# Kernel optimization log

Measured on AMD Instinct MI355X. Metric: run time of the kernel, lower is better.

Reference implementation:

```python
import jax, jax.numpy as jnp
import numpy as np

B, N, M = 8192, 64, 32          # batch, num_fields, embedding_dim
D = N * (N - 1) // 2            # 2016 pairwise-interaction rows of theta
OUT = 1024                      # block_out_dim
BN_EPS = 1e-5


def setup_inputs() -> dict:
    key = jax.random.key(0)
    k0, k1, k2, k3 = jax.random.split(key, 4)
    inputs = jax.random.normal(k0, (B, N * M), dtype=jnp.float32)
    W_z = jax.random.normal(k1, (N, N, M), dtype=jnp.float32) * 0.05
    theta = jax.random.normal(k2, (D, N), dtype=jnp.float32) * 0.05
    w_affine = jax.random.normal(k3, (OUT, N + D), dtype=jnp.float32) * 0.02
    b_affine = jnp.zeros((OUT,), dtype=jnp.float32)
    gamma = jnp.ones((OUT,), dtype=jnp.float32)
    beta = jnp.zeros((OUT,), dtype=jnp.float32)
    return {"inputs": inputs, "W_z": W_z, "theta": theta,
            "w_affine": w_affine, "b_affine": b_affine,
            "gamma": gamma, "beta": beta}


def reference(inputs, W_z, theta, w_affine, b_affine, gamma, beta):
    b = inputs.shape[0]
    x = inputs.reshape(b, N, M)                      # [B, N, M]
    # lz term: full quadratic form with W_z
    lz = jnp.einsum('bnm,dnm->bd', x, W_z)           # [B, N]
    # lp term: algebraically identical to einsum('bdnm,bdnm->bd') over
    # delta = einsum('bnm,dn->bdnm'): lp[b,d] = sum_n theta[d,n]^2 * sum_m x[b,n,m]^2
    x_sq = jnp.sum(x * x, axis=-1)                   # [B, N]
    lp = x_sq @ (theta * theta).T                    # [B, D]
    out = jnp.concatenate([lz, lp], axis=1)          # [B, N+D]
    out = out @ w_affine.T + b_affine                # [B, OUT]
    # BatchNorm1d in training mode (batch statistics, biased variance)
    mean = jnp.mean(out, axis=0)
    var = jnp.var(out, axis=0)
    out = (out - mean) * jax.lax.rsqrt(var + BN_EPS) * gamma + beta
    return out
```

## Files before the change

### kernel.cpp

```cpp
#include <hip/hip_runtime.h>
#include <stdint.h>

#define NROWS 8192
#define KX    2048
#define KA    2112
#define NF    64
#define DD    2016
#define WCOLS 2080
#define ODIM  1024
#define BN_EPS 1e-5f

#define A1_OT 32
#define A2_DC 8
#define A2_DPC 252
#define A2_OT 16

#define CONV_RPB 4
#define CONV_NB  (NROWS / CONV_RPB)
#define RED_NB   (ODIM * NF / 256)

#define A1A2_A1N 256
#define A1A2_A2E 768
#define A1A2_TOT 776

#define GBM 64
#define GBN 128
#define NT (KA / 32)

using f32x4  = __attribute__((ext_vector_type(4))) float;
using bf16x8 = __attribute__((ext_vector_type(8))) short;

__device__ __forceinline__ short f2bf(float x) {
    uint32_t u = __float_as_uint(x);
    uint32_t r = (u + 0x7FFFu + ((u >> 16) & 1u)) >> 16;
    return (short)r;
}

__device__ __forceinline__ void gload16(const void* g, void* l) {
    __builtin_amdgcn_global_load_lds(
        (const __attribute__((address_space(1))) uint32_t*)g,
        (__attribute__((address_space(3))) uint32_t*)l, 16, 0, 0);
}

#define MFMA_BF16 __builtin_amdgcn_mfma_f32_16x16x32_bf16

__global__ __launch_bounds__(256) void conv_kern(const float* __restrict__ X,
                                                 short* __restrict__ Xa,
                                                 const float* __restrict__ partials,
                                                 short* __restrict__ Aw) {
    const int t = threadIdx.x;
    const int b = blockIdx.x;
    if (b < CONV_NB) {
#pragma unroll
        for (int r = 0; r < CONV_RPB; ++r) {
            const int row = b * CONV_RPB + r;
            const float4* xr = reinterpret_cast<const float4*>(X + (size_t)row * KX);
            float4 v0 = xr[t * 2];
            float4 v1 = xr[t * 2 + 1];
            bf16x8 s;
            s[0] = f2bf(v0.x); s[1] = f2bf(v0.y); s[2] = f2bf(v0.z); s[3] = f2bf(v0.w);
            s[4] = f2bf(v1.x); s[5] = f2bf(v1.y); s[6] = f2bf(v1.z); s[7] = f2bf(v1.w);
            short* outr = Xa + (size_t)row * KA;
            reinterpret_cast<bf16x8*>(outr)[t] = s;
            float sq = v0.x*v0.x + v0.y*v0.y + v0.z*v0.z + v0.w*v0.w
                     + v1.x*v1.x + v1.y*v1.y + v1.z*v1.z + v1.w*v1.w;
            sq += __shfl_xor(sq, 1);
            sq += __shfl_xor(sq, 2);
            if ((t & 3) == 0) outr[KX + (t >> 2)] = f2bf(sq - 32.0f);
        }
    } else {
        const int idx = (b - CONV_NB) * 256 + t;
        const int o = idx >> 6, n = idx & 63;
        float s = 0.f;
#pragma unroll
        for (int c = 0; c < A2_DC; ++c)
            s += partials[((size_t)c * ODIM + o) * NF + n];
        Aw[(size_t)o * KA + KX + n] = f2bf(s);
    }
}

__global__ __launch_bounds__(256) void a1a2_kern(short* __restrict__ Aw,
                                                 const float* __restrict__ Wa,
                                                 const float* __restrict__ Wz,
                                                 const float* __restrict__ theta,
                                                 float* __restrict__ partials,
                                                 float* __restrict__ sums) {
    const int bid = blockIdx.x;
    const int t = threadIdx.x;
    __shared__ __align__(16) float smem[4096];

    if (bid >= A1A2_A2E) {
        sums[(bid - A1A2_A2E) * 256 + t] = 0.f;
        return;
    }
    if (bid < A1A2_A1N) {
        const int k = (bid & 7) * 256 + t;
        const int o0 = (bid >> 3) * A1_OT;
        for (int idx = t; idx < A1_OT * 64; idx += 256)
            smem[idx] = Wa[(size_t)(o0 + (idx >> 6)) * WCOLS + (idx & 63)];
        float wz[64];
#pragma unroll
        for (int d = 0; d < 64; ++d) wz[d] = Wz[(size_t)d * KX + k];
        __syncthreads();
#pragma unroll 2
        for (int j = 0; j < A1_OT; ++j) {
            const float* war = &smem[j * 64];
            float acc = 0.f;
#pragma unroll
            for (int d = 0; d < 64; ++d) acc += war[d] * wz[d];
            Aw[(size_t)(o0 + j) * KA + k] = f2bf(acc);
        }
    } else {
        const int b = bid - A1A2_A1N;
        const int n = t & 63;
        const int g = t >> 6;
        const int chunk = b & 7;
        const int o0 = (b >> 3) * A2_OT;
        const int d0 = chunk * A2_DPC;
        float* waT = smem;
        for (int idx = t; idx < A2_OT * A2_DPC; idx += 256) {
            const int j = idx / A2_DPC, dd = idx - j * A2_DPC;
            waT[idx] = Wa[(size_t)(o0 + j) * WCOLS + NF + d0 + dd];
        }
        __syncthreads();
        float acc[A2_OT];
#pragma unroll
        for (int j = 0; j < A2_OT; ++j) acc[j] = 0.f;
        for (int i = g; i < A2_DPC; i += 4) {
            float th = theta[(size_t)(d0 + i) * NF + n];
            float th2 = th * th;
#pragma unroll
            for (int j = 0; j < A2_OT; ++j)
                acc[j] += waT[j * A2_DPC + i] * th2;
        }
        __syncthreads();
        float* red = smem;
#pragma unroll
        for (int j = 0; j < A2_OT; ++j) red[(g * A2_OT + j) * 64 + n] = acc[j];
        __syncthreads();
#pragma unroll
        for (int k2 = 0; k2 < A2_OT * 64 / 256; ++k2) {
            const int idx = t + k2 * 256;
            const int ol = idx >> 6, nn = idx & 63;
            float s = red[(0 * A2_OT + ol) * 64 + nn] + red[(1 * A2_OT + ol) * 64 + nn]
                    + red[(2 * A2_OT + ol) * 64 + nn] + red[(3 * A2_OT + ol) * 64 + nn];
            partials[((size_t)chunk * ODIM + o0 + ol) * NF + nn] = s;
        }
    }
}

__global__ __launch_bounds__(128) void gemm_kern(const short* __restrict__ Xa,
                                                 const short* __restrict__ Aw,
                                                 float* __restrict__ C,
                                                 float* __restrict__ sums) {
    __shared__ __align__(16) short As[3][GBM * 32];
    __shared__ __align__(16) short Bs[3][GBN * 32];
    const int tid  = threadIdx.x;
    const int lane = tid & 63;
    const int wc   = tid >> 6;
    const int bm = blockIdx.x * GBM;
    const int bn = blockIdx.y * GBN;

    f32x4 acc[4][4] = {};

    const short* gA[2]; int lA[2];
#pragma unroll
    for (int i = 0; i < 2; ++i) {
        const int c = tid + i * 128;
        const int r = c >> 2, q = (c & 3) ^ ((r >> 1) & 3);
        gA[i] = Xa + (size_t)(bm + r) * KA + q * 8;
        lA[i] = c * 8;
    }
    const short* gB[4]; int lB[4];
#pragma unroll
    for (int i = 0; i < 4; ++i) {
        const int c = tid + i * 128;
        const int r = c >> 2, q = (c & 3) ^ ((r >> 1) & 3);
        gB[i] = Aw + (size_t)(bn + r) * KA + q * 8;
        lB[i] = c * 8;
    }

    const int lq = lane >> 4;
    int offA[4], offB[4];
#pragma unroll
    for (int m = 0; m < 4; ++m) {
        int ra = m * 16 + (lane & 15);
        offA[m] = ra * 32 + (lq ^ ((ra >> 1) & 3)) * 8;
        int rb = wc * 64 + m * 16 + (lane & 15);
        offB[m] = rb * 32 + (lq ^ ((rb >> 1) & 3)) * 8;
    }

#define STAGE(buf, kt) do {                         \
        const int ko_ = (kt) * 32;                  \
        gload16(gA[0] + ko_, &As[buf][lA[0]]);      \
        gload16(gA[1] + ko_, &As[buf][lA[1]]);      \
        gload16(gB[0] + ko_, &Bs[buf][lB[0]]);      \
        gload16(gB[1] + ko_, &Bs[buf][lB[1]]);      \
        gload16(gB[2] + ko_, &Bs[buf][lB[2]]);      \
        gload16(gB[3] + ko_, &Bs[buf][lB[3]]);      \
    } while (0)

#define TILE(cbuf, sbuf, kt) do {                                          \
        if ((kt) + 2 < NT) STAGE(sbuf, (kt) + 2);                          \
        bf16x8 a_[4], b_[4];                                               \
        _Pragma("unroll")                                                  \
        for (int m = 0; m < 4; ++m)                                        \
            a_[m] = *reinterpret_cast<const bf16x8*>(&As[cbuf][offA[m]]);  \
        _Pragma("unroll")                                                  \
        for (int n = 0; n < 4; ++n)                                        \
            b_[n] = *reinterpret_cast<const bf16x8*>(&Bs[cbuf][offB[n]]);  \
        asm volatile("s_waitcnt lgkmcnt(0)" ::: "memory");                 \
        __builtin_amdgcn_sched_barrier(0);                                 \
        _Pragma("unroll")                                                  \
        for (int m = 0; m < 4; ++m)                                        \
            _Pragma("unroll")                                              \
            for (int n = 0; n < 4; ++n)                                    \
                acc[m][n] = MFMA_BF16(a_[m], b_[n], acc[m][n], 0, 0, 0);   \
        if ((kt) + 2 < NT)                                                 \
            asm volatile("s_waitcnt vmcnt(6)" ::: "memory");               \
        else if ((kt) + 1 < NT)                                            \
            asm volatile("s_waitcnt vmcnt(0)" ::: "memory");               \
        __builtin_amdgcn_s_barrier();                                      \
    } while (0)

    STAGE(0, 0);
    STAGE(1, 1);
    asm volatile("s_waitcnt vmcnt(6)" ::: "memory");
    __builtin_amdgcn_s_barrier();

    for (int kt = 0; kt < NT; kt += 3) {
        TILE(0, 2, kt);
        TILE(1, 0, kt + 1);
        TILE(2, 1, kt + 2);
    }
#undef TILE
#undef STAGE

    const int rlo = (lane >> 4) * 4;
    const int cl  = lane & 15;
#pragma unroll
    for (int n = 0; n < 4; ++n) {
        const int col = bn + wc * 64 + n * 16 + cl;
        float s = 0.f, q = 0.f;
#pragma unroll
        for (int m = 0; m < 4; ++m) {
            const int rowb = bm + m * 16 + rlo;
#pragma unroll
            for (int r2 = 0; r2 < 4; ++r2) {
                float v = acc[m][n][r2];
                C[(size_t)(rowb + r2) * ODIM + col] = v;
                s += v; q += v * v;
            }
        }
        s += __shfl_xor(s, 16); s += __shfl_xor(s, 32);
        q += __shfl_xor(q, 16); q += __shfl_xor(q, 32);
        if (lane < 16) {
            atomicAdd(&sums[col], s);
            atomicAdd(&sums[ODIM + col], q);
        }
    }
}

__global__ __launch_bounds__(256) void bn_apply(float* __restrict__ C,
                                                const float* __restrict__ sums,
                                                const float* __restrict__ gamma,
                                                const float* __restrict__ beta) {
    const int g = blockIdx.x * 256 + threadIdx.x;
    const int c4 = g & (ODIM / 4 - 1);
    const int row0 = g >> 8;
    const float inv = 1.0f / (float)NROWS;
    float4 sc, sh;
    {
        float4 s0 = reinterpret_cast<const float4*>(sums)[c4];
        float4 q0 = reinterpret_cast<const float4*>(sums + ODIM)[c4];
        float4 gm = reinterpret_cast<const float4*>(gamma)[c4];
        float4 bt = reinterpret_cast<const float4*>(beta)[c4];
        float m, v;
        m = s0.x * inv; v = q0.x * inv - m * m; sc.x = gm.x * rsqrtf(v + BN_EPS); sh.x = bt.x - m * sc.x;
        m = s0.y * inv; v = q0.y * inv - m * m; sc.y = gm.y * rsqrtf(v + BN_EPS); sh.y = bt.y - m * sc.y;
        m = s0.z * inv; v = q0.z * inv - m * m; sc.z = gm.z * rsqrtf(v + BN_EPS); sh.z = bt.z - m * sc.z;
        m = s0.w * inv; v = q0.w * inv - m * m; sc.w = gm.w * rsqrtf(v + BN_EPS); sh.w = bt.w - m * sc.w;
    }
#pragma unroll
    for (int r = 0; r < 4; ++r) {
        const size_t i = (size_t)(row0 + r * 2048) * (ODIM / 4) + c4;
        float4 v = reinterpret_cast<const float4*>(C)[i];
        v.x = v.x * sc.x + sh.x;
        v.y = v.y * sc.y + sh.y;
        v.z = v.z * sc.z + sh.z;
        v.w = v.w * sc.w + sh.w;
        reinterpret_cast<float4*>(C)[i] = v;
    }
}

extern "C" void kernel_launch(void* const* d_in, const int* in_sizes, int n_in,
                              void* d_out, int out_size, void* d_ws, size_t ws_size,
                              hipStream_t stream) {
    const float* X     = (const float*)d_in[0];
    const float* Wz    = (const float*)d_in[1];
    const float* theta = (const float*)d_in[2];
    const float* Wa    = (const float*)d_in[3];
    const float* gamma = (const float*)d_in[5];
    const float* beta  = (const float*)d_in[6];
    float* out = (float*)d_out;

    char* ws = (char*)d_ws;
    float* sums = (float*)ws;
    short* Xa = (short*)(ws + 16384);
    short* Aw = (short*)(ws + 16384 + (size_t)NROWS * KA * 2);
    float* partials = (float*)(ws + 16384 + (size_t)NROWS * KA * 2
                                        + (size_t)ODIM * KA * 2);

    a1a2_kern<<<A1A2_TOT, 256, 0, stream>>>(Aw, Wa, Wz, theta, partials, sums);
    conv_kern<<<CONV_NB + RED_NB, 256, 0, stream>>>(X, Xa, partials, Aw);
    gemm_kern<<<dim3(NROWS / GBM, ODIM / GBN), 128, 0, stream>>>(Xa, Aw, out, sums);
    bn_apply<<<NROWS / 4 * ODIM / 4 / 256, 256, 0, stream>>>(out, sums, gamma, beta);
}
```

Baseline: 116.4 us.

## Enlarge GEMM block tile to 256x128x64 with 8 waves and MFMA priority

Restructures the bf16 GEMM from a 64x128 tile with 2 waves and K-step 32 into a 256x128 tile with 8 waves in a 4x2 layout and K-step 64. It uses a new XOR swizzle for the wider LDS rows and raises wave priority around the MFMA block. The aim is more operand reuse per global load, fewer barriers per K, and better latency hiding. The cost is larger LDS use (about 144KB with triple buffering), which cuts occupancy, and fewer blocks (256) to fill the GPU.

After: 100.9 us. 1.15x faster.

```diff
diff --git a/kernel.cpp b/kernel.cpp
--- a/kernel.cpp
+++ b/kernel.cpp
@@ -23,9 +23,10 @@
 #define A1A2_A2E 768
 #define A1A2_TOT 776
 
-#define GBM 64
+#define GBM 256
 #define GBN 128
-#define NT (KA / 32)
+#define GBK 64
+#define NT (KA / GBK)
 
 using f32x4  = __attribute__((ext_vector_type(4))) float;
 using bf16x8 = __attribute__((ext_vector_type(8))) short;
@@ -149,78 +150,94 @@
     }
 }
 
-__global__ __launch_bounds__(128) void gemm_kern(const short* __restrict__ Xa,
+__global__ __launch_bounds__(512) void gemm_kern(const short* __restrict__ Xa,
                                                  const short* __restrict__ Aw,
                                                  float* __restrict__ C,
                                                  float* __restrict__ sums) {
-    __shared__ __align__(16) short As[3][GBM * 32];
-    __shared__ __align__(16) short Bs[3][GBN * 32];
+    __shared__ __align__(16) short As[3][GBM * GBK];
+    __shared__ __align__(16) short Bs[3][GBN * GBK];
     const int tid  = threadIdx.x;
     const int lane = tid & 63;
-    const int wc   = tid >> 6;
+    const int cl   = lane & 15;
+    const int kq   = lane >> 4;
+    const int wid  = tid >> 6;
+    const int wr   = wid >> 1;
+    const int wc   = wid & 1;
     const int bm = blockIdx.x * GBM;
     const int bn = blockIdx.y * GBN;
 
     f32x4 acc[4][4] = {};
 
-    const short* gA[2]; int lA[2];
+    const short* gAs[4]; int ldA[4];
+#pragma unroll
+    for (int i = 0; i < 4; ++i) {
+        const int c = tid + i * 512;
+        const int row = c >> 3, cp = c & 7;
+        gAs[i] = Xa + (size_t)(bm + row) * KA + (cp ^ (row & 7)) * 8;
+        ldA[i] = c * 8;
+    }
+    const short* gBs[2]; int ldB[2];
 #pragma unroll
     for (int i = 0; i < 2; ++i) {
-        const int c = tid + i * 128;
-        const int r = c >> 2, q = (c & 3) ^ ((r >> 1) & 3);
-        gA[i] = Xa + (size_t)(bm + r) * KA + q * 8;
-        lA[i] = c * 8;
-    }
-    const short* gB[4]; int lB[4];
-#pragma unroll
-    for (int i = 0; i < 4; ++i) {
-        const int c = tid + i * 128;
-        const int r = c >> 2, q = (c & 3) ^ ((r >> 1) & 3);
-        gB[i] = Aw + (size_t)(bn + r) * KA + q * 8;
-        lB[i] = c * 8;
-    }
-
-    const int lq = lane >> 4;
-    int offA[4], offB[4];
+        const int c = tid + i * 512;
+        const int row = c >> 3, cp = c & 7;
+        gBs[i] = Aw + (size_t)(bn + row) * KA + (cp ^ (row & 7)) * 8;
+        ldB[i] = c * 8;
+    }
+
+    int offA[4][2], offB[4][2];
 #pragma unroll
     for (int m = 0; m < 4; ++m) {
-        int ra = m * 16 + (lane & 15);
-        offA[m] = ra * 32 + (lq ^ ((ra >> 1) & 3)) * 8;
-        int rb = wc * 64 + m * 16 + (lane & 15);
-        offB[m] = rb * 32 + (lq ^ ((rb >> 1) & 3)) * 8;
-    }
-
-#define STAGE(buf, kt) do {                         \
-        const int ko_ = (kt) * 32;                  \
-        gload16(gA[0] + ko_, &As[buf][lA[0]]);      \
-        gload16(gA[1] + ko_, &As[buf][lA[1]]);      \
-        gload16(gB[0] + ko_, &Bs[buf][lB[0]]);      \
-        gload16(gB[1] + ko_, &Bs[buf][lB[1]]);      \
-        gload16(gB[2] + ko_, &Bs[buf][lB[2]]);      \
-        gload16(gB[3] + ko_, &Bs[buf][lB[3]]);      \
+        const int r = wr * 64 + m * 16 + cl;
+        offA[m][0] = r * GBK + ((kq)     ^ (r & 7)) * 8;
+        offA[m][1] = r * GBK + ((4 + kq) ^ (r & 7)) * 8;
+    }
+#pragma unroll
+    for (int n = 0; n < 4; ++n) {
+        const int r = wc * 64 + n * 16 + cl;
+        offB[n][0] = r * GBK + ((kq)     ^ (r & 7)) * 8;
+        offB[n][1] = r * GBK + ((4 + kq) ^ (r & 7)) * 8;
+    }
+
+#define STAGE(buf, kt) do {                               \
+        const int ko_ = (kt) * GBK;                       \
+        gload16(gAs[0] + ko_, &As[buf][ldA[0]]);          \
+        gload16(gAs[1] + ko_, &As[buf][ldA[1]]);          \
+        gload16(gAs[2] + ko_, &As[buf][ldA[2]]);          \
+        gload16(gAs[3] + ko_, &As[buf][ldA[3]]);          \
+        gload16(gBs[0] + ko_, &Bs[buf][ldB[0]]);          \
+        gload16(gBs[1] + ko_, &Bs[buf][ldB[1]]);          \
     } while (0)
 
-#define TILE(cbuf, sbuf, kt) do {                                          \
-        if ((kt) + 2 < NT) STAGE(sbuf, (kt) + 2);                          \
-        bf16x8 a_[4], b_[4];                                               \
-        _Pragma("unroll")                                                  \
-        for (int m = 0; m < 4; ++m)                                        \
-            a_[m] = *reinterpret_cast<const bf16x8*>(&As[cbuf][offA[m]]);  \
-        _Pragma("unroll")                                                  \
-        for (int n = 0; n < 4; ++n)                                        \
-            b_[n] = *reinterpret_cast<const bf16x8*>(&Bs[cbuf][offB[n]]);  \
-        asm volatile("s_waitcnt lgkmcnt(0)" ::: "memory");                 \
-        __builtin_amdgcn_sched_barrier(0);                                 \
-        _Pragma("unroll")                                                  \
-        for (int m = 0; m < 4; ++m)                                        \
-            _Pragma("unroll")                                              \
-            for (int n = 0; n < 4; ++n)                                    \
-                acc[m][n] = MFMA_BF16(a_[m], b_[n], acc[m][n], 0, 0, 0);   \
-        if ((kt) + 2 < NT)                                                 \
-            asm volatile("s_waitcnt vmcnt(6)" ::: "memory");               \
-        else if ((kt) + 1 < NT)                                            \
-            asm volatile("s_waitcnt vmcnt(0)" ::: "memory");               \
-        __builtin_amdgcn_s_barrier();                                      \
+#define TILE(cbuf, sbuf, kt) do {                                            \
+        if ((kt) + 2 < NT) STAGE(sbuf, (kt) + 2);                            \
+        bf16x8 a_[4][2], b_[4][2];                                           \
+        _Pragma("unroll")                                                    \
+        for (int m = 0; m < 4; ++m) {                                        \
+            a_[m][0] = *reinterpret_cast<const bf16x8*>(&As[cbuf][offA[m][0]]); \
+            a_[m][1] = *reinterpret_cast<const bf16x8*>(&As[cbuf][offA[m][1]]); \
+        }                                                                    \
+        _Pragma("unroll")                                                    \
+        for (int n = 0; n < 4; ++n) {                                        \
+            b_[n][0] = *reinterpret_cast<const bf16x8*>(&Bs[cbuf][offB[n][0]]); \
+            b_[n][1] = *reinterpret_cast<const bf16x8*>(&Bs[cbuf][offB[n][1]]); \
+        }                                                                    \
+        asm volatile("s_waitcnt lgkmcnt(0)" ::: "memory");                   \
+        __builtin_amdgcn_sched_barrier(0);                                   \
+        __builtin_amdgcn_s_setprio(1);                                       \
+        _Pragma("unroll")                                                    \
+        for (int m = 0; m < 4; ++m)                                          \
+            _Pragma("unroll")                                                \
+            for (int n = 0; n < 4; ++n) {                                    \
+                acc[m][n] = MFMA_BF16(a_[m][0], b_[n][0], acc[m][n], 0, 0, 0); \
+                acc[m][n] = MFMA_BF16(a_[m][1], b_[n][1], acc[m][n], 0, 0, 0); \
+            }                                                                \
+        __builtin_amdgcn_s_setprio(0);                                       \
+        if ((kt) + 2 < NT)                                                   \
+            asm volatile("s_waitcnt vmcnt(6)" ::: "memory");                 \
+        else if ((kt) + 1 < NT)                                              \
+            asm volatile("s_waitcnt vmcnt(0)" ::: "memory");                 \
+        __builtin_amdgcn_s_barrier();                                        \
     } while (0)
 
     STAGE(0, 0);
@@ -236,15 +253,14 @@
 #undef TILE
 #undef STAGE
 
-    const int rlo = (lane >> 4) * 4;
-    const int cl  = lane & 15;
+    const int rlo = kq * 4;
 #pragma unroll
     for (int n = 0; n < 4; ++n) {
         const int col = bn + wc * 64 + n * 16 + cl;
         float s = 0.f, q = 0.f;
 #pragma unroll
         for (int m = 0; m < 4; ++m) {
-            const int rowb = bm + m * 16 + rlo;
+            const int rowb = bm + wr * 64 + m * 16 + rlo;
 #pragma unroll
             for (int r2 = 0; r2 < 4; ++r2) {
                 float v = acc[m][n][r2];
@@ -313,6 +329,6 @@
 
     a1a2_kern<<<A1A2_TOT, 256, 0, stream>>>(Aw, Wa, Wz, theta, partials, sums);
     conv_kern<<<CONV_NB + RED_NB, 256, 0, stream>>>(X, Xa, partials, Aw);
-    gemm_kern<<<dim3(NROWS / GBM, ODIM / GBN), 128, 0, stream>>>(Xa, Aw, out, sums);
+    gemm_kern<<<dim3(NROWS / GBM, ODIM / GBN), 512, 0, stream>>>(Xa, Aw, out, sums);
     bn_apply<<<NROWS / 4 * ODIM / 4 / 256, 256, 0, stream>>>(out, sums, gamma, beta);
 }
```
